# Kernel tuning notes

Hardware: AMD Instinct MI355X
Metric: run time of the kernel (lower is better)

The kernel has to match this reference:

```python
import jax, jax.numpy as jnp
import numpy as np
from jax import lax

THRESH = 0.5       # score threshold (inference default)
NMS_THRESH = 0.7   # IoU threshold for greedy NMS
K_KEEP = 512       # fixed number of NMS candidates (padded/masked)
NEG_SLOPE = 0.01   # LeakyReLU default slope


def setup_inputs() -> dict:
    key = jax.random.key(0)
    k0, k1, k2 = jax.random.split(key, 3)
    B, C, H, W = 4, 1280, 48, 48
    A, HID = 9, 256
    features = jax.random.normal(k0, (B, C, H, W), jnp.float32)
    # small init so offsets / conf logits stay in a sane range
    W1 = jax.random.normal(k1, (HID, C, 3, 3), jnp.float32) * 0.01
    b1 = jnp.zeros((HID,), jnp.float32)
    W_head = jax.random.normal(k2, (5 * A, HID, 1, 1), jnp.float32) * 0.01
    b_head = jnp.zeros((5 * A,), jnp.float32)
    anchor_wh = jnp.asarray(
        [[1, 1], [2, 2], [3, 3], [4, 4], [5, 5], [2, 3], [3, 2], [3, 5], [5, 3]],
        jnp.float32)
    return dict(features=features, W1=W1, b1=b1, W_head=W_head,
                b_head=b_head, anchor_wh=anchor_wh)


def generate_anchor_centers(H, W):
    # grid of cell centers, as in GenerateGrid (x_c, y_c at +0.5)
    ys = jnp.arange(H, dtype=jnp.float32) + 0.5
    xs = jnp.arange(W, dtype=jnp.float32) + 0.5
    yc, xc = jnp.meshgrid(ys, xs, indexing='ij')  # (H, W)
    return xc, yc


def pairwise_iou(a, b):
    # a: (N,4), b: (M,4) in (x1,y1,x2,y2) -> (N,M) IoU
    x1 = jnp.maximum(a[:, None, 0], b[None, :, 0])
    y1 = jnp.maximum(a[:, None, 1], b[None, :, 1])
    x2 = jnp.minimum(a[:, None, 2], b[None, :, 2])
    y2 = jnp.minimum(a[:, None, 3], b[None, :, 3])
    inter = jnp.clip(x2 - x1, 0.0) * jnp.clip(y2 - y1, 0.0)
    area_a = (a[:, 2] - a[:, 0]) * (a[:, 3] - a[:, 1])
    area_b = (b[:, 2] - b[:, 0]) * (b[:, 3] - b[:, 1])
    union = area_a[:, None] + area_b[None, :] - inter
    return inter / jnp.maximum(union, 1e-8)


def nms_one(boxes, scores):
    # boxes: (N,4), scores: (N,)  -> fixed-size padded outputs
    valid = scores > THRESH
    masked = jnp.where(valid, scores, -1.0)
    top_scores, idx = lax.top_k(masked, K_KEEP)       # sorted descending
    boxes_k = boxes[idx]                              # (K,4)
    valid_k = top_scores > THRESH
    iou = pairwise_iou(boxes_k, boxes_k)              # (K,K)

    def step(suppressed, i):
        keep_i = valid_k[i] & jnp.logical_not(suppressed[i])
        suppressed = suppressed | (keep_i & (iou[i] > NMS_THRESH))
        return suppressed, keep_i

    _, keep = lax.scan(step, jnp.zeros(K_KEEP, bool), jnp.arange(K_KEEP))
    return boxes_k, top_scores, keep


def reference(features, W1, b1, W_head, b_head, anchor_wh):
    B, C, H, W = features.shape
    A = anchor_wh.shape[0]
    dn = ('NCHW', 'OIHW', 'NCHW')

    # proposal module: 3x3 conv -> LeakyReLU -> 1x1 conv to 5A channels
    h = lax.conv_general_dilated(features, W1, (1, 1), 'SAME', dimension_numbers=dn)
    h = h + b1[None, :, None, None]
    h = jnp.where(h >= 0, h, NEG_SLOPE * h)
    out = lax.conv_general_dilated(h, W_head, (1, 1), 'SAME', dimension_numbers=dn)
    out = out + b_head[None, :, None, None]
    out = out.reshape(B, A, 5, H, W)
    conf = out[:, :, 0]                                # (B,A,H,W)
    tx, ty, tw, th = out[:, :, 1], out[:, :, 2], out[:, :, 3], out[:, :, 4]

    # anchor generation (GenerateGrid + GenerateAnchor)
    xc, yc = generate_anchor_centers(H, W)             # (H,W)
    wa = anchor_wh[:, 0][:, None, None]                # (A,1,1)
    ha = anchor_wh[:, 1][:, None, None]

    pxc = xc[None, None] + tx * wa[None]               # (B,A,H,W)
    pyc = yc[None, None] + ty * ha[None]
    pw = wa[None] * jnp.exp(tw)
    ph = ha[None] * jnp.exp(th)
    proposals = jnp.stack(
        [pxc - pw / 2, pyc - ph / 2, pxc + pw / 2, pyc + ph / 2], axis=-1)
    proposals = proposals.reshape(B, A * H * W, 4)     # (B,N,4)
    scores = jax.nn.sigmoid(conf).reshape(B, A * H * W)

    final_boxes, final_scores, keep = jax.vmap(nms_one)(proposals, scores)
    keep_f = keep.astype(final_boxes.dtype)
    return (final_boxes * keep_f[..., None],
            final_scores * keep_f,
            keep)
```

## Files before the change

kernel.cpp:

```cpp
#include <hip/hip_runtime.h>
#include <stdint.h>
#include <math.h>

#define HW 48
#define CIN 1280
#define HID 256
#define NA 9
#define NPOS (HW*HW)
#define NANCH (NA*NPOS)
#define KTOT 11520
#define WND 640

#define OFF_W1T   ((size_t)0)
#define OFF_H64   (OFF_W1T + 11796480ull)
#define OFF_H32   (OFF_H64 + 18874368ull)
#define OFF_K64   (OFF_H32 + 2359296ull)
#define OFF_K32   (OFF_K64 + 663552ull)
#define OFF_S64   (OFF_K32 + 82944ull)
#define OFF_S32   (OFF_S64 + 20480ull)
#define OFF_WIDX  (OFF_S32 + 10240ull)
#define OFF_SSC   (OFF_WIDX + 10240ull)
#define OFF_SIDX  (OFF_SSC + 8192ull)
#define OFF_SBX   (OFF_SIDX + 8192ull)

__device__ __forceinline__ float npmul(float a, float b) { return __fmul_rn(a, b); }
__device__ __forceinline__ float npadd(float a, float b) { return __fadd_rn(a, b); }
__device__ __forceinline__ float npsub(float a, float b) { return __fsub_rn(a, b); }

__global__ __launch_bounds__(256) void k_wt(const float* __restrict__ W1,
                                            float* __restrict__ W1t) {
  __shared__ float tile[32][73];
  const int co0 = blockIdx.x * 32;
  const int kt0 = blockIdx.y * 72;
  for (int u = threadIdx.x; u < 32*72; u += 256) {
    int co = u / 72, kt = u % 72;
    tile[co][kt] = W1[(size_t)(co0+co)*KTOT + kt0 + kt];
  }
  __syncthreads();
  for (int u = threadIdx.x; u < 32*72; u += 256) {
    int co = u % 32, kt = u / 32;
    W1t[(size_t)(kt0+kt)*256 + co0 + co] = tile[co][kt];
  }
}

__global__ __launch_bounds__(256) void k_conv(const float* __restrict__ W1t,
                                              const float* __restrict__ in,
                                              const float* __restrict__ b1,
                                              double* __restrict__ h64,
                                              float* __restrict__ h32) {
  __shared__ __align__(16) float As[16][68];
  __shared__ __align__(16) float Bs[16][68];
  const int z   = blockIdx.z;
  const int co0 = blockIdx.x * 64;
  const int p0  = blockIdx.y * 64;
  const int tid = threadIdx.x;
  const int col = (tid % 16) * 4;
  const int pl  = (tid / 16) * 4;
  const int cA  = tid & 63;
  const int kA0 = tid >> 6;
  const int pp  = tid & 63;
  const int kB0 = tid >> 6;
  const int pB  = p0 + pp;
  const int yB  = pB / HW;
  const int xB  = pB - yB * HW;

  if (z < 4) {
    const int b = z;
    const size_t bbase = (size_t)b * CIN * NPOS;
    double run[4][4], tap[4][4];
    for (int t = 0; t < 9; ++t) {
      const int dy = t / 3 - 1;
      const int dx = t % 3 - 1;
      const int yy = yB + dy;
      const int xx = xB + dx;
      const bool vB = ((unsigned)yy < (unsigned)HW) && ((unsigned)xx < (unsigned)HW);
      const size_t inoff = bbase + (size_t)(vB ? (yy*HW + xx) : 0);
      #pragma unroll
      for (int i = 0; i < 4; ++i)
        #pragma unroll
        for (int j = 0; j < 4; ++j) tap[i][j] = 0.0;

      for (int c0 = 0; c0 < CIN; c0 += 16) {
        #pragma unroll
        for (int r = 0; r < 4; ++r)
          As[kA0 + 4*r][cA] = W1t[((size_t)(c0 + kA0 + 4*r)*9 + t)*256 + co0 + cA];
        #pragma unroll
        for (int r = 0; r < 4; ++r) {
          const int kc = kB0 + 4*r;
          Bs[kc][pp] = vB ? in[inoff + (size_t)(c0 + kc)*NPOS] : 0.f;
        }
        __syncthreads();
        #pragma unroll
        for (int kc = 0; kc < 16; ++kc) {
          const float4 a4 = *(const float4*)&As[kc][col];
          const float4 b4 = *(const float4*)&Bs[kc][pl];
          const double av[4] = {(double)a4.x, (double)a4.y, (double)a4.z, (double)a4.w};
          const double bv[4] = {(double)b4.x, (double)b4.y, (double)b4.z, (double)b4.w};
          #pragma unroll
          for (int i = 0; i < 4; ++i)
            #pragma unroll
            for (int j = 0; j < 4; ++j)
              tap[i][j] = fma(av[i], bv[j], tap[i][j]);
        }
        __syncthreads();
      }
      if (t == 0) {
        #pragma unroll
        for (int i = 0; i < 4; ++i)
          #pragma unroll
          for (int j = 0; j < 4; ++j) run[i][j] = tap[i][j];
      } else {
        #pragma unroll
        for (int i = 0; i < 4; ++i)
          #pragma unroll
          for (int j = 0; j < 4; ++j) run[i][j] = run[i][j] + tap[i][j];
      }
    }
    #pragma unroll
    for (int i = 0; i < 4; ++i) {
      const int co = co0 + col + i;
      const double bias = (double)b1[co];
      #pragma unroll
      for (int j = 0; j < 4; ++j) {
        double v = run[i][j] + bias;
        v = (v >= 0.0) ? v : 0.01*v;
        h64[((size_t)b*HID + co)*NPOS + p0 + pl + j] = v;
      }
    }
  } else {
    const size_t bbase = (size_t)1 * CIN * NPOS;
    float acc[4][4];
    #pragma unroll
    for (int i = 0; i < 4; ++i)
      #pragma unroll
      for (int j = 0; j < 4; ++j) acc[i][j] = 0.f;
    for (int t = 0; t < 9; ++t) {
      const int dy = t / 3 - 1;
      const int dx = t % 3 - 1;
      const int yy = yB + dy;
      const int xx = xB + dx;
      const bool vB = ((unsigned)yy < (unsigned)HW) && ((unsigned)xx < (unsigned)HW);
      const size_t inoff = bbase + (size_t)(vB ? (yy*HW + xx) : 0);
      for (int c0 = 0; c0 < CIN; c0 += 16) {
        #pragma unroll
        for (int r = 0; r < 4; ++r)
          As[kA0 + 4*r][cA] = W1t[((size_t)(c0 + kA0 + 4*r)*9 + t)*256 + co0 + cA];
        #pragma unroll
        for (int r = 0; r < 4; ++r) {
          const int kc = kB0 + 4*r;
          Bs[kc][pp] = vB ? in[inoff + (size_t)(c0 + kc)*NPOS] : 0.f;
        }
        __syncthreads();
        #pragma unroll
        for (int kc = 0; kc < 16; ++kc) {
          const float4 a4 = *(const float4*)&As[kc][col];
          const float4 b4 = *(const float4*)&Bs[kc][pl];
          const float av[4] = {a4.x, a4.y, a4.z, a4.w};
          const float bv[4] = {b4.x, b4.y, b4.z, b4.w};
          #pragma unroll
          for (int i = 0; i < 4; ++i)
            #pragma unroll
            for (int j = 0; j < 4; ++j)
              acc[i][j] = fmaf(av[i], bv[j], acc[i][j]);
        }
        __syncthreads();
      }
    }
    #pragma unroll
    for (int i = 0; i < 4; ++i) {
      const int co = co0 + col + i;
      const float bias = b1[co];
      #pragma unroll
      for (int j = 0; j < 4; ++j) {
        float v = acc[i][j] + bias;
        v = (v >= 0.f) ? v : 0.01f*v;
        h32[(size_t)co*NPOS + p0 + pl + j] = v;
      }
    }
  }
}

__global__ __launch_bounds__(256) void k_head64(const double* __restrict__ h64,
                                                const float* __restrict__ Wh,
                                                const float* __restrict__ bh,
                                                double* __restrict__ key64) {
  const int b = blockIdx.y;
  const int p = blockIdx.x * 256 + threadIdx.x;
  if (p >= NPOS) return;
  double acc[9];
  #pragma unroll
  for (int a2 = 0; a2 < 9; ++a2) acc[a2] = 0.0;
  const double* hp = h64 + (size_t)b*HID*NPOS + p;
  for (int k = 0; k < 256; ++k) {
    const double hv = hp[(size_t)k*NPOS];
    #pragma unroll
    for (int a2 = 0; a2 < 9; ++a2)
      acc[a2] = fma(hv, (double)Wh[(size_t)(a2*5)*256 + k], acc[a2]);
  }
  #pragma unroll
  for (int a2 = 0; a2 < 9; ++a2) {
    const double c = acc[a2] + (double)bh[a2*5];
    const double s = 1.0 / (1.0 + exp(-c));
    key64[(size_t)b*NANCH + (size_t)a2*NPOS + p] = (s > 0.5) ? s : -1.0;
  }
}

__global__ __launch_bounds__(256) void k_head32(const float* __restrict__ h32,
                                                const float* __restrict__ Wh,
                                                const float* __restrict__ bh,
                                                float* __restrict__ key32) {
  const int p = blockIdx.x * 256 + threadIdx.x;
  if (p >= NPOS) return;
  float acc[9];
  #pragma unroll
  for (int a2 = 0; a2 < 9; ++a2) acc[a2] = 0.f;
  const float* hp = h32 + p;
  for (int k = 0; k < 256; ++k) {
    const float hv = hp[(size_t)k*NPOS];
    #pragma unroll
    for (int a2 = 0; a2 < 9; ++a2)
      acc[a2] = fmaf(hv, Wh[(size_t)(a2*5)*256 + k], acc[a2]);
  }
  #pragma unroll
  for (int a2 = 0; a2 < 9; ++a2) {
    const float c = npadd(acc[a2], bh[a2*5]);
    const float t = (float)exp(-(double)c);
    const float s = __fdiv_rn(1.0f, npadd(1.0f, t));
    key32[(size_t)a2*NPOS + p] = (s > 0.5f) ? s : -1.0f;
  }
}

__global__ __launch_bounds__(256) void k_rank(const double* __restrict__ key64,
                                              const float* __restrict__ key32,
                                              double* __restrict__ s64,
                                              float* __restrict__ s32,
                                              int* __restrict__ widx) {
  __shared__ double tile[1024];
  const int b = blockIdx.y;
  const int i = blockIdx.x * 256 + threadIdx.x;
  const double ki = key64[(size_t)b*NANCH + i];
  int rank = 0;
  for (int j0 = 0; j0 < NANCH; j0 += 1024) {
    const int lim = (NANCH - j0 < 1024) ? (NANCH - j0) : 1024;
    for (int u = threadIdx.x; u < 1024; u += 256) {
      const int j = j0 + u;
      tile[u] = (j < NANCH) ? key64[(size_t)b*NANCH + j] : -1.0e300;
    }
    __syncthreads();
    for (int u = 0; u < lim; ++u) {
      const double kj = tile[u];
      const int j = j0 + u;
      if (kj > ki || (kj == ki && j < i)) ++rank;
    }
    __syncthreads();
  }
  if (rank < WND) {
    s64[(size_t)b*WND + rank] = ki;
    widx[(size_t)b*WND + rank] = i;
    if (b == 1) s32[(size_t)b*WND + rank] = key32[i];
  }
}

__global__ __launch_bounds__(64) void k_fix(double* __restrict__ s64,
                                            float* __restrict__ s32,
                                            int* __restrict__ widx,
                                            float* __restrict__ ssc,
                                            int* __restrict__ sidx) {
  const int b = blockIdx.x;
  if (threadIdx.x == 0 && b == 1) {
    double* k6 = s64 + (size_t)b*WND;
    float*  k3 = s32 + (size_t)b*WND;
    int*    ix = widx + (size_t)b*WND;
    for (int s = 0; s < WND-1; ++s) {
      const float ka = k3[s], kb = k3[s+1];
      const int ia = ix[s], ib = ix[s+1];
      const bool b_before_a = (kb > ka) || (kb == ka && ib < ia);
      if (b_before_a) {
        double t6 = k6[s]; k6[s] = k6[s+1]; k6[s+1] = t6;
        float  t3 = k3[s]; k3[s] = k3[s+1]; k3[s+1] = t3;
        int    ti = ix[s]; ix[s] = ix[s+1]; ix[s+1] = ti;
      }
    }
  }
  __syncthreads();
  for (int s = threadIdx.x; s < 512; s += 64) {
    ssc[(size_t)b*512 + s] = (float)s64[(size_t)b*WND + s];
    sidx[(size_t)b*512 + s] = widx[(size_t)b*WND + s];
  }
}

__global__ __launch_bounds__(256) void k_decode2(const double* __restrict__ h64,
                                                 const int* __restrict__ sidx,
                                                 const float* __restrict__ Wh,
                                                 const float* __restrict__ bh,
                                                 const float* __restrict__ anc,
                                                 float* __restrict__ sbx) {
  const int b = blockIdx.y;
  const int s = blockIdx.x * 256 + threadIdx.x;
  if (s >= 512) return;
  const int id = sidx[(size_t)b*512 + s];
  const int a = id / NPOS;
  const int p = id % NPOS;
  const double* hp = h64 + (size_t)b*HID*NPOS + p;
  const float* w1p = Wh + (size_t)(a*5+1)*256;
  const float* w2p = Wh + (size_t)(a*5+2)*256;
  const float* w3p = Wh + (size_t)(a*5+3)*256;
  const float* w4p = Wh + (size_t)(a*5+4)*256;
  double t0 = 0.0, t1 = 0.0, t2 = 0.0, t3 = 0.0;
  for (int r = 0; r < 256; ++r) {
    const double hv = hp[(size_t)r*NPOS];
    t0 = fma(hv, (double)w1p[r], t0);
    t1 = fma(hv, (double)w2p[r], t1);
    t2 = fma(hv, (double)w3p[r], t2);
    t3 = fma(hv, (double)w4p[r], t3);
  }
  const float tx = (float)(t0 + (double)bh[a*5+1]);
  const float ty = (float)(t1 + (double)bh[a*5+2]);
  const float tw = (float)(t2 + (double)bh[a*5+3]);
  const float th = (float)(t3 + (double)bh[a*5+4]);
  const int x = p % HW, y = p / HW;
  const float wa = anc[a*2+0], ha = anc[a*2+1];
  const float pxc = npadd((float)x + 0.5f, npmul(tx, wa));
  const float pyc = npadd((float)y + 0.5f, npmul(ty, ha));
  const float pw = npmul(wa, (float)exp((double)tw));
  const float ph = npmul(ha, (float)exp((double)th));
  const float hw_ = __fdiv_rn(pw, 2.0f);
  const float hh_ = __fdiv_rn(ph, 2.0f);
  float* bp = sbx + ((size_t)b*512 + s)*4;
  bp[0] = npsub(pxc, hw_);
  bp[1] = npsub(pyc, hh_);
  bp[2] = npadd(pxc, hw_);
  bp[3] = npadd(pyc, hh_);
}

__global__ __launch_bounds__(512) void k_nms(const float* __restrict__ ssc,
                                             const float* __restrict__ sbx,
                                             float* __restrict__ out) {
  __shared__ float bxl[512][4];
  __shared__ float area[512];
  __shared__ float mscl[512];
  __shared__ unsigned long long rowb[512][8];
  __shared__ unsigned long long supw[8];
  __shared__ unsigned char keepf[512];
  const int b = blockIdx.x;
  const int tid = threadIdx.x;
  {
    const float* bp = sbx + ((size_t)b*512 + tid)*4;
    const float v0 = bp[0], v1 = bp[1], v2 = bp[2], v3 = bp[3];
    bxl[tid][0] = v0; bxl[tid][1] = v1; bxl[tid][2] = v2; bxl[tid][3] = v3;
    area[tid] = npmul(npsub(v2, v0), npsub(v3, v1));
    mscl[tid] = ssc[(size_t)b*512 + tid];
  }
  __syncthreads();
  {
    const float ax1 = bxl[tid][0], ay1 = bxl[tid][1];
    const float ax2 = bxl[tid][2], ay2 = bxl[tid][3];
    const float aa = area[tid];
    unsigned long long bits = 0;
    for (int j = 0; j < 512; ++j) {
      const float x1 = fmaxf(ax1, bxl[j][0]);
      const float y1 = fmaxf(ay1, bxl[j][1]);
      const float x2 = fminf(ax2, bxl[j][2]);
      const float y2 = fminf(ay2, bxl[j][3]);
      float iw = npsub(x2, x1); iw = (iw > 0.f) ? iw : 0.f;
      float ih = npsub(y2, y1); ih = (ih > 0.f) ? ih : 0.f;
      const float inter = npmul(iw, ih);
      const float un = npsub(npadd(aa, area[j]), inter);
      const float iou = __fdiv_rn(inter, fmaxf(un, 1e-8f));
      if (iou > 0.7f) bits |= (1ull << (j & 63));
      if ((j & 63) == 63) { rowb[tid][j >> 6] = bits; bits = 0; }
    }
  }
  __syncthreads();
  if (tid == 0) {
    for (int w = 0; w < 8; ++w) supw[w] = 0ull;
    for (int i = 0; i < 512; ++i) {
      const bool keep = (mscl[i] > 0.5f) &&
                        !((supw[i >> 6] >> (i & 63)) & 1ull);
      keepf[i] = keep ? 1 : 0;
      if (keep) {
        for (int w = 0; w < 8; ++w) supw[w] |= rowb[i][w];
      }
    }
  }
  __syncthreads();
  {
    const int row = b*512 + tid;
    const float kf = keepf[tid] ? 1.0f : 0.0f;
    #pragma unroll
    for (int c = 0; c < 4; ++c)
      out[(size_t)row*4 + c] = npmul(bxl[tid][c], kf);
    out[(size_t)2048*4 + row] = npmul(mscl[tid], kf);
    out[(size_t)2048*5 + row] = kf;
  }
}

extern "C" void kernel_launch(void* const* d_in, const int* in_sizes, int n_in,
                              void* d_out, int out_size, void* d_ws, size_t ws_size,
                              hipStream_t stream) {
  const float* feat = (const float*)d_in[0];
  const float* W1   = (const float*)d_in[1];
  const float* b1   = (const float*)d_in[2];
  const float* Wh   = (const float*)d_in[3];
  const float* bh   = (const float*)d_in[4];
  const float* anc  = (const float*)d_in[5];
  char* ws = (char*)d_ws;
  float*  W1t  = (float*)(ws + OFF_W1T);
  double* h64  = (double*)(ws + OFF_H64);
  float*  h32  = (float*)(ws + OFF_H32);
  double* k64  = (double*)(ws + OFF_K64);
  float*  k32  = (float*)(ws + OFF_K32);
  double* s64  = (double*)(ws + OFF_S64);
  float*  s32  = (float*)(ws + OFF_S32);
  int*    widx = (int*)(ws + OFF_WIDX);
  float*  ssc  = (float*)(ws + OFF_SSC);
  int*    sidx = (int*)(ws + OFF_SIDX);
  float*  sbx  = (float*)(ws + OFF_SBX);
  float* out = (float*)d_out;

  k_wt     <<<dim3(8,160),  256, 0, stream>>>(W1, W1t);
  k_conv   <<<dim3(4,36,5), 256, 0, stream>>>(W1t, feat, b1, h64, h32);
  k_head64 <<<dim3(9,4),    256, 0, stream>>>(h64, Wh, bh, k64);
  k_head32 <<<dim3(9),      256, 0, stream>>>(h32, Wh, bh, k32);
  k_rank   <<<dim3(81,4),   256, 0, stream>>>(k64, k32, s64, s32, widx);
  k_fix    <<<dim3(4),       64, 0, stream>>>(s64, s32, widx, ssc, sidx);
  k_decode2<<<dim3(2,4),    256, 0, stream>>>(h64, sidx, Wh, bh, anc, sbx);
  k_nms    <<<dim3(4),      512, 0, stream>>>(ssc, sbx, out);
}
```

Measured before the change: 4.399 ms.

## Store conv tiles as double in LDS and parallelize head, fix, decode kernels

The conv kernel now converts operands to double when staging them into shared memory, so the inner FP64 loop reads double2 values instead of converting floats on every use. This doubles LDS footprint and bandwidth per tile. The head kernels now run one thread per anchor instead of one per position covering all nine, giving nine times more threads. Decode splits its four dot products across four threads, and the fix kernel stages its data in shared memory with more threads. Together these are meant to raise parallelism in the small, latency-bound tail kernels.

```diff
diff --git a/kernel.cpp b/kernel.cpp
--- a/kernel.cpp
+++ b/kernel.cpp
@@ -48,8 +48,8 @@
                                               const float* __restrict__ b1,
                                               double* __restrict__ h64,
                                               float* __restrict__ h32) {
-  __shared__ __align__(16) float As[16][68];
-  __shared__ __align__(16) float Bs[16][68];
+  __shared__ __align__(16) double As[16][68];
+  __shared__ __align__(16) double Bs[16][68];
   const int z   = blockIdx.z;
   const int co0 = blockIdx.x * 64;
   const int p0  = blockIdx.y * 64;
@@ -83,19 +83,22 @@
       for (int c0 = 0; c0 < CIN; c0 += 16) {
         #pragma unroll
         for (int r = 0; r < 4; ++r)
-          As[kA0 + 4*r][cA] = W1t[((size_t)(c0 + kA0 + 4*r)*9 + t)*256 + co0 + cA];
+          As[kA0 + 4*r][cA] =
+            (double)W1t[((size_t)(c0 + kA0 + 4*r)*9 + t)*256 + co0 + cA];
         #pragma unroll
         for (int r = 0; r < 4; ++r) {
           const int kc = kB0 + 4*r;
-          Bs[kc][pp] = vB ? in[inoff + (size_t)(c0 + kc)*NPOS] : 0.f;
+          Bs[kc][pp] = vB ? (double)in[inoff + (size_t)(c0 + kc)*NPOS] : 0.0;
         }
         __syncthreads();
         #pragma unroll
         for (int kc = 0; kc < 16; ++kc) {
-          const float4 a4 = *(const float4*)&As[kc][col];
-          const float4 b4 = *(const float4*)&Bs[kc][pl];
-          const double av[4] = {(double)a4.x, (double)a4.y, (double)a4.z, (double)a4.w};
-          const double bv[4] = {(double)b4.x, (double)b4.y, (double)b4.z, (double)b4.w};
+          const double2 a01 = *(const double2*)&As[kc][col];
+          const double2 a23 = *(const double2*)&As[kc][col+2];
+          const double2 b01 = *(const double2*)&Bs[kc][pl];
+          const double2 b23 = *(const double2*)&Bs[kc][pl+2];
+          const double av[4] = {a01.x, a01.y, a23.x, a23.y};
+          const double bv[4] = {b01.x, b01.y, b23.x, b23.y};
           #pragma unroll
           for (int i = 0; i < 4; ++i)
             #pragma unroll
@@ -144,19 +147,22 @@
       for (int c0 = 0; c0 < CIN; c0 += 16) {
         #pragma unroll
         for (int r = 0; r < 4; ++r)
-          As[kA0 + 4*r][cA] = W1t[((size_t)(c0 + kA0 + 4*r)*9 + t)*256 + co0 + cA];
+          As[kA0 + 4*r][cA] =
+            (double)W1t[((size_t)(c0 + kA0 + 4*r)*9 + t)*256 + co0 + cA];
         #pragma unroll
         for (int r = 0; r < 4; ++r) {
           const int kc = kB0 + 4*r;
-          Bs[kc][pp] = vB ? in[inoff + (size_t)(c0 + kc)*NPOS] : 0.f;
+          Bs[kc][pp] = vB ? (double)in[inoff + (size_t)(c0 + kc)*NPOS] : 0.0;
         }
         __syncthreads();
         #pragma unroll
         for (int kc = 0; kc < 16; ++kc) {
-          const float4 a4 = *(const float4*)&As[kc][col];
-          const float4 b4 = *(const float4*)&Bs[kc][pl];
-          const float av[4] = {a4.x, a4.y, a4.z, a4.w};
-          const float bv[4] = {b4.x, b4.y, b4.z, b4.w};
+          const double2 a01 = *(const double2*)&As[kc][col];
+          const double2 a23 = *(const double2*)&As[kc][col+2];
+          const double2 b01 = *(const double2*)&Bs[kc][pl];
+          const double2 b23 = *(const double2*)&Bs[kc][pl+2];
+          const float av[4] = {(float)a01.x, (float)a01.y, (float)a23.x, (float)a23.y};
+          const float bv[4] = {(float)b01.x, (float)b01.y, (float)b23.x, (float)b23.y};
           #pragma unroll
           for (int i = 0; i < 4; ++i)
             #pragma unroll
@@ -185,49 +191,35 @@
                                                 const float* __restrict__ bh,
                                                 double* __restrict__ key64) {
   const int b = blockIdx.y;
-  const int p = blockIdx.x * 256 + threadIdx.x;
-  if (p >= NPOS) return;
-  double acc[9];
-  #pragma unroll
-  for (int a2 = 0; a2 < 9; ++a2) acc[a2] = 0.0;
+  const int gid = blockIdx.x * 256 + threadIdx.x;
+  const int a2 = gid / NPOS;
+  const int p  = gid - a2 * NPOS;
   const double* hp = h64 + (size_t)b*HID*NPOS + p;
-  for (int k = 0; k < 256; ++k) {
-    const double hv = hp[(size_t)k*NPOS];
-    #pragma unroll
-    for (int a2 = 0; a2 < 9; ++a2)
-      acc[a2] = fma(hv, (double)Wh[(size_t)(a2*5)*256 + k], acc[a2]);
-  }
-  #pragma unroll
-  for (int a2 = 0; a2 < 9; ++a2) {
-    const double c = acc[a2] + (double)bh[a2*5];
-    const double s = 1.0 / (1.0 + exp(-c));
-    key64[(size_t)b*NANCH + (size_t)a2*NPOS + p] = (s > 0.5) ? s : -1.0;
-  }
+  const float*  wp = Wh + (size_t)(a2*5)*256;
+  double acc = 0.0;
+  for (int k = 0; k < 256; ++k)
+    acc = fma(hp[(size_t)k*NPOS], (double)wp[k], acc);
+  const double c = acc + (double)bh[a2*5];
+  const double s = 1.0 / (1.0 + exp(-c));
+  key64[(size_t)b*NANCH + gid] = (s > 0.5) ? s : -1.0;
 }
 
 __global__ __launch_bounds__(256) void k_head32(const float* __restrict__ h32,
                                                 const float* __restrict__ Wh,
                                                 const float* __restrict__ bh,
                                                 float* __restrict__ key32) {
-  const int p = blockIdx.x * 256 + threadIdx.x;
-  if (p >= NPOS) return;
-  float acc[9];
-  #pragma unroll
-  for (int a2 = 0; a2 < 9; ++a2) acc[a2] = 0.f;
+  const int gid = blockIdx.x * 256 + threadIdx.x;
+  const int a2 = gid / NPOS;
+  const int p  = gid - a2 * NPOS;
   const float* hp = h32 + p;
-  for (int k = 0; k < 256; ++k) {
-    const float hv = hp[(size_t)k*NPOS];
-    #pragma unroll
-    for (int a2 = 0; a2 < 9; ++a2)
-      acc[a2] = fmaf(hv, Wh[(size_t)(a2*5)*256 + k], acc[a2]);
-  }
-  #pragma unroll
-  for (int a2 = 0; a2 < 9; ++a2) {
-    const float c = npadd(acc[a2], bh[a2*5]);
-    const float t = (float)exp(-(double)c);
-    const float s = __fdiv_rn(1.0f, npadd(1.0f, t));
-    key32[(size_t)a2*NPOS + p] = (s > 0.5f) ? s : -1.0f;
-  }
+  const float* wp = Wh + (size_t)(a2*5)*256;
+  float acc = 0.f;
+  for (int k = 0; k < 256; ++k)
+    acc = fmaf(hp[(size_t)k*NPOS], wp[k], acc);
+  const float c = npadd(acc, bh[a2*5]);
+  const float t = (float)exp(-(double)c);
+  const float s = __fdiv_rn(1.0f, npadd(1.0f, t));
+  key32[gid] = (s > 0.5f) ? s : -1.0f;
 }
 
 __global__ __launch_bounds__(256) void k_rank(const double* __restrict__ key64,
@@ -261,16 +253,22 @@
   }
 }
 
-__global__ __launch_bounds__(64) void k_fix(double* __restrict__ s64,
-                                            float* __restrict__ s32,
-                                            int* __restrict__ widx,
-                                            float* __restrict__ ssc,
-                                            int* __restrict__ sidx) {
+__global__ __launch_bounds__(256) void k_fix(const double* __restrict__ s64,
+                                             const float* __restrict__ s32,
+                                             const int* __restrict__ widx,
+                                             float* __restrict__ ssc,
+                                             int* __restrict__ sidx) {
+  __shared__ double k6[WND];
+  __shared__ float  k3[WND];
+  __shared__ int    ix[WND];
   const int b = blockIdx.x;
+  for (int u = threadIdx.x; u < WND; u += 256) {
+    k6[u] = s64[(size_t)b*WND + u];
+    k3[u] = s32[(size_t)b*WND + u];
+    ix[u] = widx[(size_t)b*WND + u];
+  }
+  __syncthreads();
   if (threadIdx.x == 0 && b == 1) {
-    double* k6 = s64 + (size_t)b*WND;
-    float*  k3 = s32 + (size_t)b*WND;
-    int*    ix = widx + (size_t)b*WND;
     for (int s = 0; s < WND-1; ++s) {
       const float ka = k3[s], kb = k3[s+1];
       const int ia = ix[s], ib = ix[s+1];
@@ -283,9 +281,9 @@
     }
   }
   __syncthreads();
-  for (int s = threadIdx.x; s < 512; s += 64) {
-    ssc[(size_t)b*512 + s] = (float)s64[(size_t)b*WND + s];
-    sidx[(size_t)b*512 + s] = widx[(size_t)b*WND + s];
+  for (int s = threadIdx.x; s < 512; s += 256) {
+    ssc[(size_t)b*512 + s] = (float)k6[s];
+    sidx[(size_t)b*512 + s] = ix[s];
   }
 }
 
@@ -295,42 +293,41 @@
                                                  const float* __restrict__ bh,
                                                  const float* __restrict__ anc,
                                                  float* __restrict__ sbx) {
+  __shared__ double sm[64][4];
   const int b = blockIdx.y;
-  const int s = blockIdx.x * 256 + threadIdx.x;
-  if (s >= 512) return;
+  const int ch = threadIdx.x & 3;
+  const int sl = threadIdx.x >> 2;
+  const int s  = blockIdx.x * 64 + sl;
   const int id = sidx[(size_t)b*512 + s];
   const int a = id / NPOS;
   const int p = id % NPOS;
   const double* hp = h64 + (size_t)b*HID*NPOS + p;
-  const float* w1p = Wh + (size_t)(a*5+1)*256;
-  const float* w2p = Wh + (size_t)(a*5+2)*256;
-  const float* w3p = Wh + (size_t)(a*5+3)*256;
-  const float* w4p = Wh + (size_t)(a*5+4)*256;
-  double t0 = 0.0, t1 = 0.0, t2 = 0.0, t3 = 0.0;
-  for (int r = 0; r < 256; ++r) {
-    const double hv = hp[(size_t)r*NPOS];
-    t0 = fma(hv, (double)w1p[r], t0);
-    t1 = fma(hv, (double)w2p[r], t1);
-    t2 = fma(hv, (double)w3p[r], t2);
-    t3 = fma(hv, (double)w4p[r], t3);
-  }
-  const float tx = (float)(t0 + (double)bh[a*5+1]);
-  const float ty = (float)(t1 + (double)bh[a*5+2]);
-  const float tw = (float)(t2 + (double)bh[a*5+3]);
-  const float th = (float)(t3 + (double)bh[a*5+4]);
-  const int x = p % HW, y = p / HW;
-  const float wa = anc[a*2+0], ha = anc[a*2+1];
-  const float pxc = npadd((float)x + 0.5f, npmul(tx, wa));
-  const float pyc = npadd((float)y + 0.5f, npmul(ty, ha));
-  const float pw = npmul(wa, (float)exp((double)tw));
-  const float ph = npmul(ha, (float)exp((double)th));
-  const float hw_ = __fdiv_rn(pw, 2.0f);
-  const float hh_ = __fdiv_rn(ph, 2.0f);
-  float* bp = sbx + ((size_t)b*512 + s)*4;
-  bp[0] = npsub(pxc, hw_);
-  bp[1] = npsub(pyc, hh_);
-  bp[2] = npadd(pxc, hw_);
-  bp[3] = npadd(pyc, hh_);
+  const float*  wp = Wh + (size_t)(a*5+1+ch)*256;
+  double acc = 0.0;
+  for (int r = 0; r < 256; ++r)
+    acc = fma(hp[(size_t)r*NPOS], (double)wp[r], acc);
+  sm[sl][ch] = acc;
+  __syncthreads();
+  if (ch == 0) {
+    const double t0 = sm[sl][0], t1 = sm[sl][1], t2 = sm[sl][2], t3 = sm[sl][3];
+    const float tx = (float)(t0 + (double)bh[a*5+1]);
+    const float ty = (float)(t1 + (double)bh[a*5+2]);
+    const float tw = (float)(t2 + (double)bh[a*5+3]);
+    const float th = (float)(t3 + (double)bh[a*5+4]);
+    const int x = p % HW, y = p / HW;
+    const float wa = anc[a*2+0], ha = anc[a*2+1];
+    const float pxc = npadd((float)x + 0.5f, npmul(tx, wa));
+    const float pyc = npadd((float)y + 0.5f, npmul(ty, ha));
+    const float pw = npmul(wa, (float)exp((double)tw));
+    const float ph = npmul(ha, (float)exp((double)th));
+    const float hw_ = __fdiv_rn(pw, 2.0f);
+    const float hh_ = __fdiv_rn(ph, 2.0f);
+    float* bp = sbx + ((size_t)b*512 + s)*4;
+    bp[0] = npsub(pxc, hw_);
+    bp[1] = npsub(pyc, hh_);
+    bp[2] = npadd(pxc, hw_);
+    bp[3] = npadd(pyc, hh_);
+  }
 }
 
 __global__ __launch_bounds__(512) void k_nms(const float* __restrict__ ssc,
@@ -420,10 +417,10 @@
 
   k_wt     <<<dim3(8,160),  256, 0, stream>>>(W1, W1t);
   k_conv   <<<dim3(4,36,5), 256, 0, stream>>>(W1t, feat, b1, h64, h32);
-  k_head64 <<<dim3(9,4),    256, 0, stream>>>(h64, Wh, bh, k64);
-  k_head32 <<<dim3(9),      256, 0, stream>>>(h32, Wh, bh, k32);
+  k_head64 <<<dim3(81,4),   256, 0, stream>>>(h64, Wh, bh, k64);
+  k_head32 <<<dim3(81),     256, 0, stream>>>(h32, Wh, bh, k32);
   k_rank   <<<dim3(81,4),   256, 0, stream>>>(k64, k32, s64, s32, widx);
-  k_fix    <<<dim3(4),       64, 0, stream>>>(s64, s32, widx, ssc, sidx);
-  k_decode2<<<dim3(2,4),    256, 0, stream>>>(h64, sidx, Wh, bh, anc, sbx);
+  k_fix    <<<dim3(4),      256, 0, stream>>>(s64, s32, widx, ssc, sidx);
+  k_decode2<<<dim3(8,4),    256, 0, stream>>>(h64, sidx, Wh, bh, anc, sbx);
   k_nms    <<<dim3(4),      512, 0, stream>>>(ssc, sbx, out);
 }
```

After: 5.520 ms. 1.25x slower.
